# Kernel tuning notes

Hardware: AMD Instinct MI355X
Metric: run time of the kernel (lower is better)

Reference implementation:

```python
import jax, jax.numpy as jnp
from jax import lax
import numpy as np

B, H, W, C = 8, 56, 56, 384
NUM_HEADS, HEAD_CH = 6, 64
BN_EPS = 1e-5
DN = ('NHWC', 'HWIO', 'NHWC')


def conv_proj(x, dw_kernel, bn_scale, bn_bias, bn_mean, bn_var, pw_kernel, stride):
    """Depthwise conv -> BatchNorm (eval) -> 1x1 pointwise conv, all SAME padding."""
    in_ch = x.shape[-1]
    x = lax.conv_general_dilated(x, dw_kernel, (stride, stride), 'SAME',
                                 dimension_numbers=DN, feature_group_count=in_ch)
    x = (x - bn_mean) * (bn_scale / jnp.sqrt(bn_var + BN_EPS)) + bn_bias
    x = lax.conv_general_dilated(x, pw_kernel, (1, 1), 'SAME', dimension_numbers=DN)
    return x


def setup_inputs() -> dict:
    key = jax.random.key(0)
    ks = jax.random.split(key, 16)
    d = {
        'inputs_q': jax.random.normal(ks[0], (B, H, W, C), jnp.float32),
        'inputs_kv': jax.random.normal(ks[1], (B, H, W, C), jnp.float32),
        'out_kernel': jax.random.normal(ks[2], (NUM_HEADS, HEAD_CH, C), jnp.float32) * 0.05,
    }
    for i, p in enumerate(['q', 'k', 'v']):
        d[f'{p}_dw_kernel'] = jax.random.normal(ks[3 + i], (3, 3, 1, C), jnp.float32) * 0.1
        d[f'{p}_bn_scale'] = jnp.ones((C,), jnp.float32)
        d[f'{p}_bn_bias'] = jnp.zeros((C,), jnp.float32)
        d[f'{p}_bn_mean'] = jnp.zeros((C,), jnp.float32)
        d[f'{p}_bn_var'] = jnp.ones((C,), jnp.float32)
        d[f'{p}_pw_kernel'] = jax.random.normal(ks[6 + i], (1, 1, C, NUM_HEADS * HEAD_CH), jnp.float32) * 0.05
    return d


def reference(inputs_q, inputs_kv,
              q_dw_kernel, q_bn_scale, q_bn_bias, q_bn_mean, q_bn_var, q_pw_kernel,
              k_dw_kernel, k_bn_scale, k_bn_bias, k_bn_mean, k_bn_var, k_pw_kernel,
              v_dw_kernel, v_bn_scale, v_bn_bias, v_bn_mean, v_bn_var, v_pw_kernel,
              out_kernel):
    q = conv_proj(inputs_q, q_dw_kernel, q_bn_scale, q_bn_bias, q_bn_mean, q_bn_var, q_pw_kernel, 1)
    k = conv_proj(inputs_kv, k_dw_kernel, k_bn_scale, k_bn_bias, k_bn_mean, k_bn_var, k_pw_kernel, 2)
    v = conv_proj(inputs_kv, v_dw_kernel, v_bn_scale, v_bn_bias, v_bn_mean, v_bn_var, v_pw_kernel, 2)

    def to_tokens(x):  # [b,H,W,h*d] -> [b,HW,h,d]
        b, hh, ww, _ = x.shape
        return x.reshape(b, hh * ww, NUM_HEADS, HEAD_CH)

    q = to_tokens(q) / jnp.sqrt(jnp.float32(HEAD_CH))
    k = to_tokens(k)
    v = to_tokens(v)

    attn = jnp.einsum('bqhd,bkhd->bhqk', q, k)       # [b,h,Nq,Nkv]
    attn = jax.nn.softmax(attn, axis=-1)
    out = jnp.einsum('bhqk,bkhd->bqhd', attn, v)     # [b,Nq,h,d]
    out = jnp.einsum('bqhd,hdo->bqo', out, out_kernel)  # DenseGeneral over (h,d)
    return out
```

## Files before the change

### kernel.cpp

```cpp
#include <hip/hip_runtime.h>
#include <hip/hip_bf16.h>
#include <hip/hip_fp16.h>

#define BB 8
#define HH 56
#define WW 56
#define CC 384
#define NHD 6
#define DD 64
#define HK 28
#define WK 28
#define NQ (HH*WW)
#define NKV (HK*WK)
#define NTOK (BB*NQ)
#define NTOKKV (BB*NKV)
#define BN_EPS 1e-5f
#define LOG2E 1.44269504f

typedef _Float16 f16;
typedef _Float16 f16x2 __attribute__((ext_vector_type(2)));
typedef _Float16 f16x4 __attribute__((ext_vector_type(4)));
typedef _Float16 f16x8 __attribute__((ext_vector_type(8)));
typedef float f32x4 __attribute__((ext_vector_type(4)));

__device__ __forceinline__ float fast_exp2(float x) {
#if __has_builtin(__builtin_amdgcn_exp2f)
  return __builtin_amdgcn_exp2f(x);
#else
  return __expf(x * 0.69314718056f);
#endif
}

__device__ __forceinline__ f16x4 pack4(float p0, float p1, float p2, float p3) {
#if __has_builtin(__builtin_amdgcn_cvt_pkrtz)
  f16x2 a = __builtin_bit_cast(f16x2, __builtin_amdgcn_cvt_pkrtz(p0, p1));
  f16x2 b = __builtin_bit_cast(f16x2, __builtin_amdgcn_cvt_pkrtz(p2, p3));
  return __builtin_shufflevector(a, b, 0, 1, 2, 3);
#else
  f16x4 r; r[0] = (f16)p0; r[1] = (f16)p1; r[2] = (f16)p2; r[3] = (f16)p3;
  return r;
#endif
}

__device__ __forceinline__ void dw_s1_body(
    int blk, int tid, const float* __restrict__ in, const float* __restrict__ w,
    const float* __restrict__ bns, const float* __restrict__ bnb,
    const float* __restrict__ bnm, const float* __restrict__ bnv,
    f16* __restrict__ out) {
  int idx = blk * 256 + tid;
  int pp = idx / 96;
  int c = (idx % 96) * 4;
  int b = pp / (HH * WK);
  int rem = pp % (HH * WK);
  int y = rem / WK, xh = rem % WK;
  int x0 = xh * 2;
  float a0x = 0, a0y = 0, a0z = 0, a0w = 0;
  float a1x = 0, a1y = 0, a1z = 0, a1w = 0;
#pragma unroll
  for (int kh = 0; kh < 3; ++kh) {
    int iy = y + kh - 1;
    if ((unsigned)iy >= (unsigned)HH) continue;
    const float* rp = in + ((size_t)(b * HH + iy) * WW) * CC + c;
    const float4 z4 = {0.f, 0.f, 0.f, 0.f};
    const float4 v0 = (x0 > 0) ? *(const float4*)(rp + (size_t)(x0 - 1) * CC) : z4;
    const float4 v1 = *(const float4*)(rp + (size_t)x0 * CC);
    const float4 v2 = *(const float4*)(rp + (size_t)(x0 + 1) * CC);
    const float4 v3 = (x0 < 54) ? *(const float4*)(rp + (size_t)(x0 + 2) * CC) : z4;
    const float4 w0 = *(const float4*)(w + (kh * 3 + 0) * CC + c);
    const float4 w1 = *(const float4*)(w + (kh * 3 + 1) * CC + c);
    const float4 w2 = *(const float4*)(w + (kh * 3 + 2) * CC + c);
    a0x = fmaf(v0.x, w0.x, fmaf(v1.x, w1.x, fmaf(v2.x, w2.x, a0x)));
    a0y = fmaf(v0.y, w0.y, fmaf(v1.y, w1.y, fmaf(v2.y, w2.y, a0y)));
    a0z = fmaf(v0.z, w0.z, fmaf(v1.z, w1.z, fmaf(v2.z, w2.z, a0z)));
    a0w = fmaf(v0.w, w0.w, fmaf(v1.w, w1.w, fmaf(v2.w, w2.w, a0w)));
    a1x = fmaf(v1.x, w0.x, fmaf(v2.x, w1.x, fmaf(v3.x, w2.x, a1x)));
    a1y = fmaf(v1.y, w0.y, fmaf(v2.y, w1.y, fmaf(v3.y, w2.y, a1y)));
    a1z = fmaf(v1.z, w0.z, fmaf(v2.z, w1.z, fmaf(v3.z, w2.z, a1z)));
    a1w = fmaf(v1.w, w0.w, fmaf(v2.w, w1.w, fmaf(v3.w, w2.w, a1w)));
  }
  const float4 s = *(const float4*)(bns + c);
  const float4 bi = *(const float4*)(bnb + c);
  const float4 m = *(const float4*)(bnm + c);
  const float4 va = *(const float4*)(bnv + c);
  f16x4 r0, r1;
  float g;
  g = s.x * rsqrtf(va.x + BN_EPS); r0[0] = (f16)fmaf(a0x - m.x, g, bi.x); r1[0] = (f16)fmaf(a1x - m.x, g, bi.x);
  g = s.y * rsqrtf(va.y + BN_EPS); r0[1] = (f16)fmaf(a0y - m.y, g, bi.y); r1[1] = (f16)fmaf(a1y - m.y, g, bi.y);
  g = s.z * rsqrtf(va.z + BN_EPS); r0[2] = (f16)fmaf(a0z - m.z, g, bi.z); r1[2] = (f16)fmaf(a1z - m.z, g, bi.z);
  g = s.w * rsqrtf(va.w + BN_EPS); r0[3] = (f16)fmaf(a0w - m.w, g, bi.w); r1[3] = (f16)fmaf(a1w - m.w, g, bi.w);
  const size_t pix0 = (size_t)b * NQ + y * WW + x0;
  *(f16x4*)(out + pix0 * CC + c) = r0;
  *(f16x4*)(out + (pix0 + 1) * CC + c) = r1;
}

__device__ __forceinline__ void dw_s2_body(
    int blk, int tid, const float* __restrict__ in,
    const float* __restrict__ wk_, const float* __restrict__ kbs, const float* __restrict__ kbb,
    const float* __restrict__ kbm, const float* __restrict__ kbv,
    const float* __restrict__ wv_, const float* __restrict__ vbs, const float* __restrict__ vbb,
    const float* __restrict__ vbm, const float* __restrict__ vbv,
    f16* __restrict__ outk, f16* __restrict__ outv) {
  int idx = blk * 256 + tid;
  int pix = idx / 96;
  int c = (idx % 96) * 4;
  int b = pix / (HK * WK);
  int p = pix % (HK * WK);
  int oy = p / WK, ox = p % WK;
  float kx = 0, ky = 0, kz = 0, kw4 = 0;
  float vx = 0, vy = 0, vz = 0, vw4 = 0;
#pragma unroll
  for (int kh = 0; kh < 3; ++kh) {
    int iy = oy * 2 + kh;
    if (iy >= HH) continue;
#pragma unroll
    for (int kwi = 0; kwi < 3; ++kwi) {
      int ix = ox * 2 + kwi;
      if (ix >= WW) continue;
      const float4 v = *(const float4*)(in + (((size_t)(b * HH + iy) * WW + ix) * CC + c));
      const float4 a = *(const float4*)(wk_ + ((kh * 3 + kwi) * CC + c));
      const float4 bq = *(const float4*)(wv_ + ((kh * 3 + kwi) * CC + c));
      kx = fmaf(v.x, a.x, kx); ky = fmaf(v.y, a.y, ky);
      kz = fmaf(v.z, a.z, kz); kw4 = fmaf(v.w, a.w, kw4);
      vx = fmaf(v.x, bq.x, vx); vy = fmaf(v.y, bq.y, vy);
      vz = fmaf(v.z, bq.z, vz); vw4 = fmaf(v.w, bq.w, vw4);
    }
  }
  {
    const float4 s = *(const float4*)(kbs + c);
    const float4 bi = *(const float4*)(kbb + c);
    const float4 m = *(const float4*)(kbm + c);
    const float4 va = *(const float4*)(kbv + c);
    f16x4 r; float g;
    g = s.x * rsqrtf(va.x + BN_EPS); r[0] = (f16)fmaf(kx - m.x, g, bi.x);
    g = s.y * rsqrtf(va.y + BN_EPS); r[1] = (f16)fmaf(ky - m.y, g, bi.y);
    g = s.z * rsqrtf(va.z + BN_EPS); r[2] = (f16)fmaf(kz - m.z, g, bi.z);
    g = s.w * rsqrtf(va.w + BN_EPS); r[3] = (f16)fmaf(kw4 - m.w, g, bi.w);
    *(f16x4*)(outk + (size_t)pix * CC + c) = r;
  }
  {
    const float4 s = *(const float4*)(vbs + c);
    const float4 bi = *(const float4*)(vbb + c);
    const float4 m = *(const float4*)(vbm + c);
    const float4 va = *(const float4*)(vbv + c);
    f16x4 r; float g;
    g = s.x * rsqrtf(va.x + BN_EPS); r[0] = (f16)fmaf(vx - m.x, g, bi.x);
    g = s.y * rsqrtf(va.y + BN_EPS); r[1] = (f16)fmaf(vy - m.y, g, bi.y);
    g = s.z * rsqrtf(va.z + BN_EPS); r[2] = (f16)fmaf(vz - m.z, g, bi.z);
    g = s.w * rsqrtf(va.w + BN_EPS); r[3] = (f16)fmaf(vw4 - m.w, g, bi.w);
    *(f16x4*)(outv + (size_t)pix * CC + c) = r;
  }
}

__global__ __launch_bounds__(256) void preprocess(
    const float* __restrict__ inputs_q, const float* __restrict__ inputs_kv,
    const float* __restrict__ q_dwk, const float* __restrict__ q_bs,
    const float* __restrict__ q_bb, const float* __restrict__ q_bm,
    const float* __restrict__ q_bv,
    const float* __restrict__ k_dwk, const float* __restrict__ k_bs,
    const float* __restrict__ k_bb, const float* __restrict__ k_bm,
    const float* __restrict__ k_bv,
    const float* __restrict__ v_dwk, const float* __restrict__ v_bs,
    const float* __restrict__ v_bb, const float* __restrict__ v_bm,
    const float* __restrict__ v_bv,
    const float* __restrict__ w0, const float* __restrict__ w1,
    const float* __restrict__ w2, const float* __restrict__ w3,
    f16* __restrict__ o0, f16* __restrict__ o1,
    f16* __restrict__ o2, f16* __restrict__ o3,
    f16* __restrict__ qdw, f16* __restrict__ kdw, f16* __restrict__ vdw) {
  __shared__ float t[32][33];
  const int blk = blockIdx.x;
  const int tid = threadIdx.x;
  if (blk < 4704) {
    dw_s1_body(blk, tid, inputs_q, q_dwk, q_bs, q_bb, q_bm, q_bv, qdw);
  } else if (blk < 7056) {
    dw_s2_body(blk - 4704, tid, inputs_kv,
               k_dwk, k_bs, k_bb, k_bm, k_bv,
               v_dwk, v_bs, v_bb, v_bm, v_bv, kdw, vdw);
  } else {
    const int r = blk - 7056;
    const int z = r / 144, rem = r % 144;
    const int bx = rem % 12, by = rem / 12;
    const float* src = z == 0 ? w0 : z == 1 ? w1 : z == 2 ? w2 : w3;
    f16* dst = z == 0 ? o0 : z == 1 ? o1 : z == 2 ? o2 : o3;
    const int k0 = bx * 32, n0 = by * 32;
    const int x = tid & 31, y = tid >> 5;
#pragma unroll
    for (int i = 0; i < 4; ++i) t[y + i * 8][x] = src[(size_t)(k0 + y + i * 8) * 384 + n0 + x];
    __syncthreads();
#pragma unroll
    for (int i = 0; i < 4; ++i)
      dst[(size_t)(n0 + y + i * 8) * 384 + k0 + x] = (f16)t[x][y + i * 8];
  }
}

template <int MODE>
__device__ __forceinline__ void gemm_body(
    const f16* __restrict__ A, const f16* __restrict__ Bt,
    float* __restrict__ Cf, f16* __restrict__ Ch, float scale,
    int row0, int col0) {
  __shared__ f16 As[128 * 32];
  __shared__ f16 Bs[128 * 32];
  const int tid = threadIdx.x;
  const int wave = tid >> 6, lane = tid & 63;
  const int c = lane & 15, g = lane >> 4;
  const int wr = wave >> 1, wc = wave & 1;

  f32x4 acc[4][4] = {};

  for (int k0 = 0; k0 < 384; k0 += 32) {
    __syncthreads();
#pragma unroll
    for (int ph = 0; ph < 2; ++ph) {
      const int i = ph * 256 + wave * 64 + lane;
      const f16* sa = A + (size_t)(row0 + (i >> 2)) * 384 + k0 + (i & 3) * 8;
      __builtin_amdgcn_global_load_lds(
          (const __attribute__((address_space(1))) void*)sa,
          (__attribute__((address_space(3))) void*)(As + ph * 2048 + wave * 512), 16, 0, 0);
      const f16* sb = Bt + (size_t)(col0 + (i >> 2)) * 384 + k0 + (i & 3) * 8;
      __builtin_amdgcn_global_load_lds(
          (const __attribute__((address_space(1))) void*)sb,
          (__attribute__((address_space(3))) void*)(Bs + ph * 2048 + wave * 512), 16, 0, 0);
    }
    __syncthreads();

    f16x8 bf[4];
#pragma unroll
    for (int n = 0; n < 4; ++n)
      bf[n] = *(const f16x8*)(Bs + (size_t)(wc * 64 + n * 16 + c) * 32 + g * 8);
#pragma unroll
    for (int m = 0; m < 4; ++m) {
      f16x8 af = *(const f16x8*)(As + (size_t)(wr * 64 + m * 16 + c) * 32 + g * 8);
#pragma unroll
      for (int n = 0; n < 4; ++n)
        acc[m][n] = __builtin_amdgcn_mfma_f32_16x16x32_f16(af, bf[n], acc[m][n], 0, 0, 0);
    }
  }

  if (MODE == 2) {
#pragma unroll
    for (int m = 0; m < 4; ++m)
#pragma unroll
      for (int n = 0; n < 4; ++n) {
        const int gr = row0 + wr * 64 + m * 16 + g * 4;
        const int col = col0 + wc * 64 + n * 16 + c;
        const int bb = gr / NKV;
        const int kv = gr - bb * NKV;
        f16x4 pk;
#pragma unroll
        for (int r = 0; r < 4; ++r) pk[r] = (f16)(acc[m][n][r] * scale);
        *(f16x4*)(Ch + ((size_t)bb * 384 + col) * NKV + kv) = pk;
      }
  } else {
#pragma unroll
    for (int m = 0; m < 4; ++m)
#pragma unroll
      for (int n = 0; n < 4; ++n)
#pragma unroll
        for (int r = 0; r < 4; ++r) {
          const size_t row = row0 + wr * 64 + m * 16 + g * 4 + r;
          const size_t col = col0 + wc * 64 + n * 16 + c;
          if (MODE == 1) Ch[row * 384 + col] = (f16)(acc[m][n][r] * scale);
          else           Cf[row * 384 + col] = acc[m][n][r] * scale;
        }
  }
}

__global__ __launch_bounds__(256) void gemm_qkv(
    const f16* __restrict__ qdw, const f16* __restrict__ wqt, f16* __restrict__ qf, float qscale,
    const f16* __restrict__ kdw, const f16* __restrict__ wkt, f16* __restrict__ kf,
    const f16* __restrict__ vdw, const f16* __restrict__ wvt, f16* __restrict__ vtp) {
  const int blk = blockIdx.x;
  if (blk < 588) {
    gemm_body<1>(qdw, wqt, nullptr, qf, qscale, (blk % 196) * 128, (blk / 196) * 128);
  } else if (blk < 735) {
    const int r = blk - 588;
    gemm_body<1>(kdw, wkt, nullptr, kf, 1.0f, (r % 49) * 128, (r / 49) * 128);
  } else {
    const int r = blk - 735;
    gemm_body<2>(vdw, wvt, nullptr, vtp, 1.0f, (r % 49) * 128, (r / 49) * 128);
  }
}

template <int MODE>
__global__ __launch_bounds__(256) void gemm_mfma(
    const f16* __restrict__ A, const f16* __restrict__ Bt,
    float* __restrict__ Cf, f16* __restrict__ Ch, float scale) {
  gemm_body<MODE>(A, Bt, Cf, Ch, scale, blockIdx.x * 128, blockIdx.y * 128);
}

__device__ __forceinline__ void softmax_tile(
    f32x4 (&s)[4], float& mrun, f32x4 (&o)[4], f32x4& osum,
    f16* __restrict__ pq, int c, int g) {
  float mt = s[0][0];
#pragma unroll
  for (int ct = 0; ct < 4; ++ct)
#pragma unroll
    for (int r = 0; r < 4; ++r) mt = fmaxf(mt, s[ct][r]);
  mt = fmaxf(mt, __shfl_xor(mt, 16));
  mt = fmaxf(mt, __shfl_xor(mt, 32));
  if (__ballot(mt > mrun + 8.0f)) {
    const float mnew = fmaxf(mrun, mt);
    const float corr = fast_exp2(mrun - mnew);
    mrun = mnew;
#pragma unroll
    for (int r = 0; r < 4; ++r) {
      const float co = __shfl(corr, g * 4 + r);
#pragma unroll
      for (int dt = 0; dt < 4; ++dt) o[dt][r] *= co;
      osum[r] *= co;
    }
  }
#pragma unroll
  for (int ct = 0; ct < 4; ++ct) {
    const float p0 = fast_exp2(s[ct][0] - mrun);
    const float p1 = fast_exp2(s[ct][1] - mrun);
    const float p2 = fast_exp2(s[ct][2] - mrun);
    const float p3 = fast_exp2(s[ct][3] - mrun);
    const int sch = (ct * 2 + (g >> 1)) ^ (c & 7);
    *(f16x4*)(pq + c * 64 + sch * 8 + (g & 1) * 4) = pack4(p0, p1, p2, p3);
  }
}

__global__ __launch_bounds__(256) void attn_mfma(
    const f16* __restrict__ qp, const f16* __restrict__ kp,
    const f16* __restrict__ vt, f16* __restrict__ op) {
  __shared__ f16 Ks[64 * 64];
  __shared__ f16 Vs[64 * 64];
  __shared__ f16 Ps[4][32 * 64];
  const int bid = blockIdx.x;
  const int qt = bid % 25;
  const int bh = bid / 25;
  const int h = bh % NHD, b = bh / NHD;
  const int tid = threadIdx.x;
  const int wave = tid >> 6, lane = tid & 63;
  const int c = lane & 15, g = lane >> 4;

  const int qr0 = qt * 128 + wave * 16 + c;
  int qr1 = qt * 128 + 64 + wave * 16 + c;
  if (qr1 > NQ - 1) qr1 = NQ - 1;
  const f16* qpb = qp + (size_t)b * NQ * 384 + h * 64;
  f16x8 qa[2][2];
  qa[0][0] = *(const f16x8*)(qpb + (size_t)qr0 * 384 + g * 8);
  qa[0][1] = *(const f16x8*)(qpb + (size_t)qr0 * 384 + 32 + g * 8);
  qa[1][0] = *(const f16x8*)(qpb + (size_t)qr1 * 384 + g * 8);
  qa[1][1] = *(const f16x8*)(qpb + (size_t)qr1 * 384 + 32 + g * 8);

  f16x8 vones;
#pragma unroll
  for (int j = 0; j < 8; ++j) vones[j] = (f16)1.0f;

  const int tid8 = tid >> 3, tch = tid & 7;
  const int lch = tch ^ (tid8 & 7);

  const f16* kbase = kp + (size_t)b * NKV * 384 + h * 64;
  const f16* vbase = vt + ((size_t)(b * 384 + h * 64)) * NKV;

  float mrun0 = -1e30f, mrun1 = -1e30f;
  f32x4 o0[4] = {}, o1[4] = {};
  f32x4 osum0 = {}, osum1 = {};
  f16* prow = &Ps[wave][0];

  for (int t0 = 0; t0 < NKV; t0 += 64) {
    __syncthreads();
    {
      int kv0 = t0 + tid8; if (kv0 > NKV - 1) kv0 = NKV - 1;
      int kv1 = t0 + 32 + tid8; if (kv1 > NKV - 1) kv1 = NKV - 1;
      __builtin_amdgcn_global_load_lds(
          (const __attribute__((address_space(1))) void*)(kbase + (size_t)kv0 * 384 + lch * 8),
          (__attribute__((address_space(3))) void*)(Ks + wave * 512), 16, 0, 0);
      __builtin_amdgcn_global_load_lds(
          (const __attribute__((address_space(1))) void*)(kbase + (size_t)kv1 * 384 + lch * 8),
          (__attribute__((address_space(3))) void*)(Ks + 2048 + wave * 512), 16, 0, 0);
      int col = t0 + lch * 8; if (col > NKV - 8) col = NKV - 8;
      __builtin_amdgcn_global_load_lds(
          (const __attribute__((address_space(1))) void*)(vbase + (size_t)tid8 * NKV + col),
          (__attribute__((address_space(3))) void*)(Vs + wave * 512), 16, 0, 0);
      __builtin_amdgcn_global_load_lds(
          (const __attribute__((address_space(1))) void*)(vbase + (size_t)(32 + tid8) * NKV + col),
          (__attribute__((address_space(3))) void*)(Vs + 2048 + wave * 512), 16, 0, 0);
    }
    __syncthreads();

    f32x4 s0[4] = {}, s1[4] = {};
#pragma unroll
    for (int kh = 0; kh < 2; ++kh) {
#pragma unroll
      for (int ct = 0; ct < 4; ++ct) {
        const int row = ct * 16 + c;
        const int sch = (kh * 4 + g) ^ (row & 7);
        f16x8 kb = *(const f16x8*)(Ks + row * 64 + sch * 8);
        s0[ct] = __builtin_amdgcn_mfma_f32_16x16x32_f16(kb, qa[0][kh], s0[ct], 0, 0, 0);
        s1[ct] = __builtin_amdgcn_mfma_f32_16x16x32_f16(kb, qa[1][kh], s1[ct], 0, 0, 0);
      }
    }
    if (t0 + 64 > NKV) {
#pragma unroll
      for (int ct = 0; ct < 4; ++ct)
#pragma unroll
        for (int r = 0; r < 4; ++r)
          if (t0 + ct * 16 + g * 4 + r >= NKV) { s0[ct][r] = -1e30f; s1[ct][r] = -1e30f; }
    }

    softmax_tile(s0, mrun0, o0, osum0, prow, c, g);
    softmax_tile(s1, mrun1, o1, osum1, prow + 16 * 64, c, g);

#pragma unroll
    for (int ks = 0; ks < 2; ++ks) {
      const int sp = (ks * 4 + g) ^ (c & 7);
      f16x8 pa0 = *(const f16x8*)(prow + c * 64 + sp * 8);
      f16x8 pa1 = *(const f16x8*)(prow + (16 + c) * 64 + sp * 8);
#pragma unroll
      for (int dt = 0; dt < 4; ++dt) {
        const int d = dt * 16 + c;
        f16x8 vb = *(const f16x8*)(Vs + d * 64 + sp * 8);
        o0[dt] = __builtin_amdgcn_mfma_f32_16x16x32_f16(pa0, vb, o0[dt], 0, 0, 0);
        o1[dt] = __builtin_amdgcn_mfma_f32_16x16x32_f16(pa1, vb, o1[dt], 0, 0, 0);
      }
      osum0 = __builtin_amdgcn_mfma_f32_16x16x32_f16(pa0, vones, osum0, 0, 0, 0);
      osum1 = __builtin_amdgcn_mfma_f32_16x16x32_f16(pa1, vones, osum1, 0, 0, 0);
    }
  }

  f16* ob0 = op + ((size_t)(b * NQ + qt * 128 + wave * 16)) * 384 + h * 64;
#pragma unroll
  for (int r = 0; r < 4; ++r) {
    const float iv = 1.0f / osum0[r];
#pragma unroll
    for (int dt = 0; dt < 4; ++dt)
      ob0[(size_t)(g * 4 + r) * 384 + dt * 16 + c] = (f16)(o0[dt][r] * iv);
  }
  if (qt != 24) {
    f16* ob1 = op + ((size_t)(b * NQ + qt * 128 + 64 + wave * 16)) * 384 + h * 64;
#pragma unroll
    for (int r = 0; r < 4; ++r) {
      const float iv = 1.0f / osum1[r];
#pragma unroll
      for (int dt = 0; dt < 4; ++dt)
        ob1[(size_t)(g * 4 + r) * 384 + dt * 16 + c] = (f16)(o1[dt][r] * iv);
    }
  }
}

extern "C" void kernel_launch(void* const* d_in, const int* in_sizes, int n_in,
                              void* d_out, int out_size, void* d_ws, size_t ws_size,
                              hipStream_t stream) {
  const float* inputs_q  = (const float*)d_in[0];
  const float* inputs_kv = (const float*)d_in[1];
  const float* out_kern  = (const float*)d_in[2];
  const float* q_dwk = (const float*)d_in[3];
  const float* q_bs  = (const float*)d_in[4];
  const float* q_bb  = (const float*)d_in[5];
  const float* q_bm  = (const float*)d_in[6];
  const float* q_bv  = (const float*)d_in[7];
  const float* q_pwk = (const float*)d_in[8];
  const float* k_dwk = (const float*)d_in[9];
  const float* k_bs  = (const float*)d_in[10];
  const float* k_bb  = (const float*)d_in[11];
  const float* k_bm  = (const float*)d_in[12];
  const float* k_bv  = (const float*)d_in[13];
  const float* k_pwk = (const float*)d_in[14];
  const float* v_dwk = (const float*)d_in[15];
  const float* v_bs  = (const float*)d_in[16];
  const float* v_bb  = (const float*)d_in[17];
  const float* v_bm  = (const float*)d_in[18];
  const float* v_bv  = (const float*)d_in[19];
  const float* v_pwk = (const float*)d_in[20];

  char* wsb = (char*)d_ws;
  f16* qdw = (f16*)(wsb + 0);
  f16* kdw = (f16*)(wsb + 19267584);
  f16* vdw = (f16*)(wsb + 24084480);
  f16* qf  = (f16*)(wsb + 28901376);
  f16* kf  = (f16*)(wsb + 48168960);
  f16* vtp = (f16*)(wsb + 57802752);
  f16* of  = (f16*)(wsb + 62619648);
  f16* wqt = (f16*)(wsb + 81887232);
  f16* wkt = (f16*)(wsb + 82182144);
  f16* wvt = (f16*)(wsb + 82477056);
  f16* wot = (f16*)(wsb + 82771968);

  preprocess<<<7632, 256, 0, stream>>>(
      inputs_q, inputs_kv,
      q_dwk, q_bs, q_bb, q_bm, q_bv,
      k_dwk, k_bs, k_bb, k_bm, k_bv,
      v_dwk, v_bs, v_bb, v_bm, v_bv,
      q_pwk, k_pwk, v_pwk, out_kern, wqt, wkt, wvt, wot,
      qdw, kdw, vdw);
  gemm_qkv<<<882, 256, 0, stream>>>(qdw, wqt, qf, 0.125f * LOG2E,
                                    kdw, wkt, kf, vdw, wvt, vtp);
  attn_mfma<<<BB * NHD * 25, 256, 0, stream>>>(qf, kf, vtp, of);
  gemm_mfma<0><<<dim3(196, 3), 256, 0, stream>>>(of, wot, (float*)d_out, nullptr, 1.0f);
}
```

Baseline: 164.8 us.

## Halve attention query tile per block, deepen GEMM K-step with swizzled LDS

The attention kernel now gives each block 64 query rows instead of 128 (one 16-row tile per wave), launching 2352 blocks instead of 1200. The aim is better occupancy and load balance, since 3136 queries divide evenly into 49 tiles, at the cost of loading each K/V tile twice as often. The GEMM body doubles its K step to 64 and uses an XOR-swizzled LDS layout, which halves the number of barriers and is meant to cut LDS bank conflicts. s_setprio hints are also placed around the MFMA sections of attention.

```diff
diff --git a/kernel.cpp b/kernel.cpp
--- a/kernel.cpp
+++ b/kernel.cpp
@@ -198,41 +198,50 @@
     const f16* __restrict__ A, const f16* __restrict__ Bt,
     float* __restrict__ Cf, f16* __restrict__ Ch, float scale,
     int row0, int col0) {
-  __shared__ f16 As[128 * 32];
-  __shared__ f16 Bs[128 * 32];
+  __shared__ f16 As[128 * 64];
+  __shared__ f16 Bs[128 * 64];
   const int tid = threadIdx.x;
   const int wave = tid >> 6, lane = tid & 63;
   const int c = lane & 15, g = lane >> 4;
   const int wr = wave >> 1, wc = wave & 1;
 
+  const int s_base = wave * 64 + lane;
   f32x4 acc[4][4] = {};
 
-  for (int k0 = 0; k0 < 384; k0 += 32) {
+  for (int k0 = 0; k0 < 384; k0 += 64) {
     __syncthreads();
 #pragma unroll
-    for (int ph = 0; ph < 2; ++ph) {
-      const int i = ph * 256 + wave * 64 + lane;
-      const f16* sa = A + (size_t)(row0 + (i >> 2)) * 384 + k0 + (i & 3) * 8;
+    for (int j = 0; j < 4; ++j) {
+      const int s = j * 256 + s_base;
+      const int row = s >> 3, sch = s & 7;
+      const int lch = sch ^ (row & 7);
+      const f16* sa = A + (size_t)(row0 + row) * 384 + k0 + lch * 8;
       __builtin_amdgcn_global_load_lds(
           (const __attribute__((address_space(1))) void*)sa,
-          (__attribute__((address_space(3))) void*)(As + ph * 2048 + wave * 512), 16, 0, 0);
-      const f16* sb = Bt + (size_t)(col0 + (i >> 2)) * 384 + k0 + (i & 3) * 8;
+          (__attribute__((address_space(3))) void*)(As + j * 2048 + wave * 512), 16, 0, 0);
+      const f16* sb = Bt + (size_t)(col0 + row) * 384 + k0 + lch * 8;
       __builtin_amdgcn_global_load_lds(
           (const __attribute__((address_space(1))) void*)sb,
-          (__attribute__((address_space(3))) void*)(Bs + ph * 2048 + wave * 512), 16, 0, 0);
+          (__attribute__((address_space(3))) void*)(Bs + j * 2048 + wave * 512), 16, 0, 0);
     }
     __syncthreads();
 
-    f16x8 bf[4];
-#pragma unroll
-    for (int n = 0; n < 4; ++n)
-      bf[n] = *(const f16x8*)(Bs + (size_t)(wc * 64 + n * 16 + c) * 32 + g * 8);
-#pragma unroll
-    for (int m = 0; m < 4; ++m) {
-      f16x8 af = *(const f16x8*)(As + (size_t)(wr * 64 + m * 16 + c) * 32 + g * 8);
-#pragma unroll
-      for (int n = 0; n < 4; ++n)
-        acc[m][n] = __builtin_amdgcn_mfma_f32_16x16x32_f16(af, bf[n], acc[m][n], 0, 0, 0);
+#pragma unroll
+    for (int kh = 0; kh < 2; ++kh) {
+      f16x8 bf[4];
+#pragma unroll
+      for (int n = 0; n < 4; ++n) {
+        const int row = wc * 64 + n * 16 + c;
+        bf[n] = *(const f16x8*)(Bs + (size_t)row * 64 + ((kh * 4 + g) ^ (row & 7)) * 8);
+      }
+#pragma unroll
+      for (int m = 0; m < 4; ++m) {
+        const int row = wr * 64 + m * 16 + c;
+        f16x8 af = *(const f16x8*)(As + (size_t)row * 64 + ((kh * 4 + g) ^ (row & 7)) * 8);
+#pragma unroll
+        for (int n = 0; n < 4; ++n)
+          acc[m][n] = __builtin_amdgcn_mfma_f32_16x16x32_f16(af, bf[n], acc[m][n], 0, 0, 0);
+      }
     }
   }
 
@@ -288,62 +297,24 @@
   gemm_body<MODE>(A, Bt, Cf, Ch, scale, blockIdx.x * 128, blockIdx.y * 128);
 }
 
-__device__ __forceinline__ void softmax_tile(
-    f32x4 (&s)[4], float& mrun, f32x4 (&o)[4], f32x4& osum,
-    f16* __restrict__ pq, int c, int g) {
-  float mt = s[0][0];
-#pragma unroll
-  for (int ct = 0; ct < 4; ++ct)
-#pragma unroll
-    for (int r = 0; r < 4; ++r) mt = fmaxf(mt, s[ct][r]);
-  mt = fmaxf(mt, __shfl_xor(mt, 16));
-  mt = fmaxf(mt, __shfl_xor(mt, 32));
-  if (__ballot(mt > mrun + 8.0f)) {
-    const float mnew = fmaxf(mrun, mt);
-    const float corr = fast_exp2(mrun - mnew);
-    mrun = mnew;
-#pragma unroll
-    for (int r = 0; r < 4; ++r) {
-      const float co = __shfl(corr, g * 4 + r);
-#pragma unroll
-      for (int dt = 0; dt < 4; ++dt) o[dt][r] *= co;
-      osum[r] *= co;
-    }
-  }
-#pragma unroll
-  for (int ct = 0; ct < 4; ++ct) {
-    const float p0 = fast_exp2(s[ct][0] - mrun);
-    const float p1 = fast_exp2(s[ct][1] - mrun);
-    const float p2 = fast_exp2(s[ct][2] - mrun);
-    const float p3 = fast_exp2(s[ct][3] - mrun);
-    const int sch = (ct * 2 + (g >> 1)) ^ (c & 7);
-    *(f16x4*)(pq + c * 64 + sch * 8 + (g & 1) * 4) = pack4(p0, p1, p2, p3);
-  }
-}
-
 __global__ __launch_bounds__(256) void attn_mfma(
     const f16* __restrict__ qp, const f16* __restrict__ kp,
     const f16* __restrict__ vt, f16* __restrict__ op) {
   __shared__ f16 Ks[64 * 64];
   __shared__ f16 Vs[64 * 64];
-  __shared__ f16 Ps[4][32 * 64];
+  __shared__ f16 Ps[4][16 * 64];
   const int bid = blockIdx.x;
-  const int qt = bid % 25;
-  const int bh = bid / 25;
+  const int qt = bid % 49;
+  const int bh = bid / 49;
   const int h = bh % NHD, b = bh / NHD;
   const int tid = threadIdx.x;
   const int wave = tid >> 6, lane = tid & 63;
   const int c = lane & 15, g = lane >> 4;
 
-  const int qr0 = qt * 128 + wave * 16 + c;
-  int qr1 = qt * 128 + 64 + wave * 16 + c;
-  if (qr1 > NQ - 1) qr1 = NQ - 1;
-  const f16* qpb = qp + (size_t)b * NQ * 384 + h * 64;
-  f16x8 qa[2][2];
-  qa[0][0] = *(const f16x8*)(qpb + (size_t)qr0 * 384 + g * 8);
-  qa[0][1] = *(const f16x8*)(qpb + (size_t)qr0 * 384 + 32 + g * 8);
-  qa[1][0] = *(const f16x8*)(qpb + (size_t)qr1 * 384 + g * 8);
-  qa[1][1] = *(const f16x8*)(qpb + (size_t)qr1 * 384 + 32 + g * 8);
+  const size_t qrow = (size_t)b * NQ + qt * 64 + wave * 16 + c;
+  f16x8 qa[2];
+  qa[0] = *(const f16x8*)(qp + qrow * 384 + h * 64 + g * 8);
+  qa[1] = *(const f16x8*)(qp + qrow * 384 + h * 64 + 32 + g * 8);
 
   f16x8 vones;
 #pragma unroll
@@ -352,12 +323,12 @@
   const int tid8 = tid >> 3, tch = tid & 7;
   const int lch = tch ^ (tid8 & 7);
 
-  const f16* kbase = kp + (size_t)b * NKV * 384 + h * 64;
+  const f16* kbase = kp + ((size_t)b * NKV) * 384 + h * 64;
   const f16* vbase = vt + ((size_t)(b * 384 + h * 64)) * NKV;
 
-  float mrun0 = -1e30f, mrun1 = -1e30f;
-  f32x4 o0[4] = {}, o1[4] = {};
-  f32x4 osum0 = {}, osum1 = {};
+  float mrun = -1e30f;
+  f32x4 o[4] = {};
+  f32x4 osum = {};
   f16* prow = &Ps[wave][0];
 
   for (int t0 = 0; t0 < NKV; t0 += 64) {
@@ -381,7 +352,8 @@
     }
     __syncthreads();
 
-    f32x4 s0[4] = {}, s1[4] = {};
+    f32x4 s[4] = {};
+    __builtin_amdgcn_s_setprio(1);
 #pragma unroll
     for (int kh = 0; kh < 2; ++kh) {
 #pragma unroll
@@ -389,55 +361,72 @@
         const int row = ct * 16 + c;
         const int sch = (kh * 4 + g) ^ (row & 7);
         f16x8 kb = *(const f16x8*)(Ks + row * 64 + sch * 8);
-        s0[ct] = __builtin_amdgcn_mfma_f32_16x16x32_f16(kb, qa[0][kh], s0[ct], 0, 0, 0);
-        s1[ct] = __builtin_amdgcn_mfma_f32_16x16x32_f16(kb, qa[1][kh], s1[ct], 0, 0, 0);
-      }
-    }
+        s[ct] = __builtin_amdgcn_mfma_f32_16x16x32_f16(kb, qa[kh], s[ct], 0, 0, 0);
+      }
+    }
+    __builtin_amdgcn_s_setprio(0);
     if (t0 + 64 > NKV) {
 #pragma unroll
       for (int ct = 0; ct < 4; ++ct)
 #pragma unroll
         for (int r = 0; r < 4; ++r)
-          if (t0 + ct * 16 + g * 4 + r >= NKV) { s0[ct][r] = -1e30f; s1[ct][r] = -1e30f; }
-    }
-
-    softmax_tile(s0, mrun0, o0, osum0, prow, c, g);
-    softmax_tile(s1, mrun1, o1, osum1, prow + 16 * 64, c, g);
-
+          if (t0 + ct * 16 + g * 4 + r >= NKV) s[ct][r] = -1e30f;
+    }
+
+    float mt = s[0][0];
+#pragma unroll
+    for (int ct = 0; ct < 4; ++ct)
+#pragma unroll
+      for (int r = 0; r < 4; ++r) mt = fmaxf(mt, s[ct][r]);
+    mt = fmaxf(mt, __shfl_xor(mt, 16));
+    mt = fmaxf(mt, __shfl_xor(mt, 32));
+
+    if (__ballot(mt > mrun + 8.0f)) {
+      const float mnew = fmaxf(mrun, mt);
+      const float corr = fast_exp2(mrun - mnew);
+      mrun = mnew;
+#pragma unroll
+      for (int r = 0; r < 4; ++r) {
+        const float co = __shfl(corr, g * 4 + r);
+#pragma unroll
+        for (int dt = 0; dt < 4; ++dt) o[dt][r] *= co;
+        osum[r] *= co;
+      }
+    }
+
+#pragma unroll
+    for (int ct = 0; ct < 4; ++ct) {
+      const float p0 = fast_exp2(s[ct][0] - mrun);
+      const float p1 = fast_exp2(s[ct][1] - mrun);
+      const float p2 = fast_exp2(s[ct][2] - mrun);
+      const float p3 = fast_exp2(s[ct][3] - mrun);
+      const int sch = (ct * 2 + (g >> 1)) ^ (c & 7);
+      *(f16x4*)(prow + c * 64 + sch * 8 + (g & 1) * 4) = pack4(p0, p1, p2, p3);
+    }
+
+    __builtin_amdgcn_s_setprio(1);
 #pragma unroll
     for (int ks = 0; ks < 2; ++ks) {
       const int sp = (ks * 4 + g) ^ (c & 7);
-      f16x8 pa0 = *(const f16x8*)(prow + c * 64 + sp * 8);
-      f16x8 pa1 = *(const f16x8*)(prow + (16 + c) * 64 + sp * 8);
+      f16x8 pa = *(const f16x8*)(prow + c * 64 + sp * 8);
 #pragma unroll
       for (int dt = 0; dt < 4; ++dt) {
         const int d = dt * 16 + c;
         f16x8 vb = *(const f16x8*)(Vs + d * 64 + sp * 8);
-        o0[dt] = __builtin_amdgcn_mfma_f32_16x16x32_f16(pa0, vb, o0[dt], 0, 0, 0);
-        o1[dt] = __builtin_amdgcn_mfma_f32_16x16x32_f16(pa1, vb, o1[dt], 0, 0, 0);
-      }
-      osum0 = __builtin_amdgcn_mfma_f32_16x16x32_f16(pa0, vones, osum0, 0, 0, 0);
-      osum1 = __builtin_amdgcn_mfma_f32_16x16x32_f16(pa1, vones, osum1, 0, 0, 0);
-    }
-  }
-
-  f16* ob0 = op + ((size_t)(b * NQ + qt * 128 + wave * 16)) * 384 + h * 64;
+        o[dt] = __builtin_amdgcn_mfma_f32_16x16x32_f16(pa, vb, o[dt], 0, 0, 0);
+      }
+      osum = __builtin_amdgcn_mfma_f32_16x16x32_f16(pa, vones, osum, 0, 0, 0);
+    }
+    __builtin_amdgcn_s_setprio(0);
+  }
+
+  f16* obase = op + ((size_t)(b * NQ + qt * 64 + wave * 16)) * 384 + h * 64;
 #pragma unroll
   for (int r = 0; r < 4; ++r) {
-    const float iv = 1.0f / osum0[r];
+    const float iv = 1.0f / osum[r];
 #pragma unroll
     for (int dt = 0; dt < 4; ++dt)
-      ob0[(size_t)(g * 4 + r) * 384 + dt * 16 + c] = (f16)(o0[dt][r] * iv);
-  }
-  if (qt != 24) {
-    f16* ob1 = op + ((size_t)(b * NQ + qt * 128 + 64 + wave * 16)) * 384 + h * 64;
-#pragma unroll
-    for (int r = 0; r < 4; ++r) {
-      const float iv = 1.0f / osum1[r];
-#pragma unroll
-      for (int dt = 0; dt < 4; ++dt)
-        ob1[(size_t)(g * 4 + r) * 384 + dt * 16 + c] = (f16)(o1[dt][r] * iv);
-    }
+      obase[(size_t)(g * 4 + r) * 384 + dt * 16 + c] = (f16)(o[dt][r] * iv);
   }
 }
 
@@ -488,6 +477,6 @@
       qdw, kdw, vdw);
   gemm_qkv<<<882, 256, 0, stream>>>(qdw, wqt, qf, 0.125f * LOG2E,
                                     kdw, wkt, kf, vdw, wvt, vtp);
-  attn_mfma<<<BB * NHD * 25, 256, 0, stream>>>(qf, kf, vtp, of);
+  attn_mfma<<<BB * NHD * 49, 256, 0, stream>>>(qf, kf, vtp, of);
   gemm_mfma<0><<<dim3(196, 3), 256, 0, stream>>>(of, wot, (float*)d_out, nullptr, 1.0f);
 }
```

Result: faster. 153.7 us (-6.7%).
